# Kernel optimization log

Hardware: AMD Instinct MI355X
Metric: run time of the kernel (lower is better)

## Reference

```python
import jax, jax.numpy as jnp
import numpy as np

B, C, T, H, NCLS = 512, 22, 1000, 64, 4


def setup_inputs() -> dict:
    key = jax.random.key(0)
    ks = jax.random.split(key, 8)
    s_ih = 1.0 / np.sqrt(H)
    x = jax.random.normal(ks[0], (B, C, T), dtype=jnp.float32)
    # PyTorch LSTM params: gate order [i, f, g, o], each of size H
    W_ih = jax.random.uniform(ks[1], (4 * H, C), minval=-s_ih, maxval=s_ih, dtype=jnp.float32)
    W_hh = jax.random.uniform(ks[2], (4 * H, H), minval=-s_ih, maxval=s_ih, dtype=jnp.float32)
    b_ih = jax.random.uniform(ks[3], (4 * H,), minval=-s_ih, maxval=s_ih, dtype=jnp.float32)
    b_hh = jax.random.uniform(ks[4], (4 * H,), minval=-s_ih, maxval=s_ih, dtype=jnp.float32)
    s_fc = 1.0 / np.sqrt(H * T)
    W_fc = jax.random.uniform(ks[5], (NCLS, H * T), minval=-s_fc, maxval=s_fc, dtype=jnp.float32)
    b_fc = jax.random.uniform(ks[6], (NCLS,), minval=-s_fc, maxval=s_fc, dtype=jnp.float32)
    return {"x": x, "W_ih": W_ih, "W_hh": W_hh, "b_ih": b_ih, "b_hh": b_hh,
            "W_fc": W_fc, "b_fc": b_fc}


def _lstm(xs, W_ih, W_hh, b_ih, b_hh):
    # xs: [B, T, C] -> outputs [B, T, H]
    b = xs.shape[0]
    # precompute input projections for all timesteps: [T, B, 4H]
    x_proj = jnp.einsum('btc,gc->tbg', xs, W_ih) + (b_ih + b_hh)
    h0 = jnp.zeros((b, W_hh.shape[1]), xs.dtype)
    c0 = jnp.zeros_like(h0)

    def step(carry, xp):
        h, c = carry
        gates = xp + h @ W_hh.T  # [B, 4H]
        i, f, g, o = jnp.split(gates, 4, axis=-1)
        i = jax.nn.sigmoid(i)
        f = jax.nn.sigmoid(f)
        g = jnp.tanh(g)
        o = jax.nn.sigmoid(o)
        c = f * c + i * g
        h = o * jnp.tanh(c)
        return (h, c), h

    _, hs = jax.lax.scan(step, (h0, c0), x_proj)  # hs: [T, B, H]
    return jnp.transpose(hs, (1, 0, 2))  # [B, T, H]


def reference(x, W_ih, W_hh, b_ih, b_hh, W_fc, b_fc):
    xs = jnp.transpose(x, (0, 2, 1))  # [B, T, C]  (permute(0,2,1))
    hs = _lstm(xs, W_ih, W_hh, b_ih, b_hh)  # [B, T, H]
    flat = hs.reshape(hs.shape[0], -1)  # [B, T*H], time-major per row
    logits = flat @ W_fc.T + b_fc  # [B, 4]
    return jax.nn.softmax(logits, axis=1)
```

## Files before the change

### kernel.cpp

```cpp
#include <hip/hip_runtime.h>

#define BB   512
#define CC   22
#define TT   1000
#define HH   64
#define NCLS 4
#define TC   250
#define NCHUNK (TT / TC)
#define XROW 12

typedef _Float16 f16;
typedef __attribute__((ext_vector_type(2))) _Float16 h2;

__device__ __forceinline__ float sigm(float x) {
    return 1.0f / (1.0f + __expf(-x));
}
__device__ __forceinline__ float tanh_(float x) {
    float e = __expf(-2.0f * fabsf(x));
    float r = (1.0f - e) / (1.0f + e);
    return copysignf(r, x);
}

__device__ __forceinline__ h2 u2h(unsigned u) {
    union { unsigned u; h2 h; } c; c.u = u; return c.h;
}
__device__ __forceinline__ unsigned h2u(h2 h) {
    union { unsigned u; h2 h; } c; c.h = h; return c.u;
}

__global__ __launch_bounds__(64, 1) void lstm_wave(
    const float* __restrict__ x,
    const float* __restrict__ W_ih,
    const float* __restrict__ W_hh,
    const float* __restrict__ b_ih,
    const float* __restrict__ b_hh,
    const float* __restrict__ W_fc,
    const float* __restrict__ b_fc,
    float* __restrict__ out)
{
    __shared__ __align__(16) h2  xs[TC][XROW];
    __shared__ __align__(16) f16 hbuf[HH];

    const int lane = threadIdx.x;
    const int r    = blockIdx.x;

    unsigned whh[4][32];
    unsigned wih[4][11];
    float bias[4];
    #pragma unroll
    for (int g = 0; g < 4; ++g) {
        const int row = g * HH + lane;
        const float* wr = W_hh + row * HH;
        #pragma unroll
        for (int k = 0; k < 32; ++k)
            whh[g][k] = h2u(h2{(f16)wr[2 * k], (f16)wr[2 * k + 1]});
        const float* wi = W_ih + row * CC;
        #pragma unroll
        for (int k = 0; k < 11; ++k)
            wih[g][k] = h2u(h2{(f16)wi[2 * k], (f16)wi[2 * k + 1]});
        bias[g] = b_ih[row] + b_hh[row];
    }
    #pragma unroll
    for (int g = 0; g < 4; ++g) {
        #pragma unroll
        for (int k = 0; k < 32; ++k) asm volatile("" : "+v"(whh[g][k]));
        #pragma unroll
        for (int k = 0; k < 11; ++k) asm volatile("" : "+v"(wih[g][k]));
        asm volatile("" : "+v"(bias[g]));
    }

    hbuf[lane] = (f16)0.0f;
    float c = 0.0f;
    float fc0 = 0.f, fc1 = 0.f, fc2 = 0.f, fc3 = 0.f;
    const float* p0 = W_fc + 0 * (TT * HH) + lane;
    const float* p1 = W_fc + 1 * (TT * HH) + lane;
    const float* p2 = W_fc + 2 * (TT * HH) + lane;
    const float* p3 = W_fc + 3 * (TT * HH) + lane;
    const float* xrow = x + (size_t)r * (CC * TT);

    for (int chunk = 0; chunk < NCHUNK; ++chunk) {
        for (int tb = 0; tb < TC; tb += 64) {
            const int t = tb + lane;
            if (t < TC) {
                const float* gx = xrow + chunk * TC + t;
                union { h2 h[XROW]; uint4 q[3]; } U;
                #pragma unroll
                for (int k = 0; k < 11; ++k)
                    U.h[k] = h2{(f16)gx[(2 * k) * TT], (f16)gx[(2 * k + 1) * TT]};
                U.h[11] = h2{(f16)0.0f, (f16)0.0f};
                uint4* dst = (uint4*)&xs[t][0];
                dst[0] = U.q[0]; dst[1] = U.q[1]; dst[2] = U.q[2];
            }
        }

        for (int tt = 0; tt < TC; ++tt) {
            union { uint4 q[8]; h2 h[32]; } H;
            const uint4* hr = (const uint4*)hbuf;
            #pragma unroll
            for (int i = 0; i < 8; ++i) H.q[i] = hr[i];

            union { uint4 q[3]; h2 h[XROW]; } X;
            const uint4* xr = (const uint4*)&xs[tt][0];
            X.q[0] = xr[0]; X.q[1] = xr[1]; X.q[2] = xr[2];

            float w0 = *p0, w1 = *p1, w2 = *p2, w3 = *p3;
            p0 += HH; p1 += HH; p2 += HH; p3 += HH;

            float a0 = bias[0], a1 = bias[1], a2 = bias[2], a3 = bias[3];
            #pragma unroll
            for (int k = 0; k < 11; ++k) {
                a0 = __builtin_amdgcn_fdot2(X.h[k], u2h(wih[0][k]), a0, false);
                a1 = __builtin_amdgcn_fdot2(X.h[k], u2h(wih[1][k]), a1, false);
                a2 = __builtin_amdgcn_fdot2(X.h[k], u2h(wih[2][k]), a2, false);
                a3 = __builtin_amdgcn_fdot2(X.h[k], u2h(wih[3][k]), a3, false);
            }
            #pragma unroll
            for (int k = 0; k < 32; ++k) {
                a0 = __builtin_amdgcn_fdot2(H.h[k], u2h(whh[0][k]), a0, false);
                a1 = __builtin_amdgcn_fdot2(H.h[k], u2h(whh[1][k]), a1, false);
                a2 = __builtin_amdgcn_fdot2(H.h[k], u2h(whh[2][k]), a2, false);
                a3 = __builtin_amdgcn_fdot2(H.h[k], u2h(whh[3][k]), a3, false);
            }

            float iv = sigm(a0), fv = sigm(a1), gv = tanh_(a2), ov = sigm(a3);
            c = fv * c + iv * gv;
            float h = ov * tanh_(c);

            fc0 += h * w0; fc1 += h * w1; fc2 += h * w2; fc3 += h * w3;

            hbuf[lane] = (f16)h;
        }
    }

    #pragma unroll
    for (int off = 32; off; off >>= 1) {
        fc0 += __shfl_down(fc0, off);
        fc1 += __shfl_down(fc1, off);
        fc2 += __shfl_down(fc2, off);
        fc3 += __shfl_down(fc3, off);
    }
    if (lane == 0) {
        float l0 = fc0 + b_fc[0], l1 = fc1 + b_fc[1];
        float l2 = fc2 + b_fc[2], l3 = fc3 + b_fc[3];
        float m  = fmaxf(fmaxf(l0, l1), fmaxf(l2, l3));
        float e0 = __expf(l0 - m), e1 = __expf(l1 - m);
        float e2 = __expf(l2 - m), e3 = __expf(l3 - m);
        float s  = e0 + e1 + e2 + e3;
        float4 o; o.x = e0 / s; o.y = e1 / s; o.z = e2 / s; o.w = e3 / s;
        *(float4*)(out + r * NCLS) = o;
    }
}

extern "C" void kernel_launch(void* const* d_in, const int* in_sizes, int n_in,
                              void* d_out, int out_size, void* d_ws, size_t ws_size,
                              hipStream_t stream) {
    const float* x    = (const float*)d_in[0];
    const float* W_ih = (const float*)d_in[1];
    const float* W_hh = (const float*)d_in[2];
    const float* b_ih = (const float*)d_in[3];
    const float* b_hh = (const float*)d_in[4];
    const float* W_fc = (const float*)d_in[5];
    const float* b_fc = (const float*)d_in[6];
    float* out = (float*)d_out;

    lstm_wave<<<BB, 64, 0, stream>>>(x, W_ih, W_hh, b_ih, b_hh, W_fc, b_fc, out);
}
```

Measured before the change: 681.1 us.

## Batch 16 sequences per block and compute LSTM gates with MFMA

Replaces the one-wave-per-sequence fdot2 kernel with 256-thread blocks, each handling 16 batch rows. The gate matmul (W_hh and W_ih concatenated as K=96) runs as 16x16x32 f16 MFMAs, with h exchanged through double-buffered LDS and a block barrier every timestep. It also swaps divides for rcp in the activations and reduces the FC partials across waves via LDS. Only 32 blocks are launched, so most CUs sit idle, and the per-step __syncthreads adds latency to the serial recurrence.

```diff
diff --git a/kernel.cpp b/kernel.cpp
--- a/kernel.cpp
+++ b/kernel.cpp
@@ -5,30 +5,35 @@
 #define TT   1000
 #define HH   64
 #define NCLS 4
-#define TC   250
+#define RPB  16
+#define NBLK (BB / RPB)
+#define TC   50
 #define NCHUNK (TT / TC)
-#define XROW 12
+#define FCW  (TT * HH)
 
 typedef _Float16 f16;
 typedef __attribute__((ext_vector_type(2))) _Float16 h2;
+typedef __attribute__((ext_vector_type(8))) _Float16 f16x8;
+typedef __attribute__((ext_vector_type(4))) float    f32x4;
+
+union U16x8 { uint4 q; f16x8 h; f16 e[8]; };
 
 __device__ __forceinline__ float sigm(float x) {
-    return 1.0f / (1.0f + __expf(-x));
+    float e = __expf(-x);
+    return __builtin_amdgcn_rcpf(1.0f + e);
 }
 __device__ __forceinline__ float tanh_(float x) {
     float e = __expf(-2.0f * fabsf(x));
-    float r = (1.0f - e) / (1.0f + e);
+    float r = (1.0f - e) * __builtin_amdgcn_rcpf(1.0f + e);
     return copysignf(r, x);
 }
-
-__device__ __forceinline__ h2 u2h(unsigned u) {
-    union { unsigned u; h2 h; } c; c.u = u; return c.h;
-}
-__device__ __forceinline__ unsigned h2u(h2 h) {
-    union { unsigned u; h2 h; } c; c.h = h; return c.u;
-}
-
-__global__ __launch_bounds__(64, 1) void lstm_wave(
+__device__ __forceinline__ unsigned pack2(float a, float b) {
+    union { unsigned u; h2 h; } c;
+    c.h = h2{(f16)a, (f16)b};
+    return c.u;
+}
+
+__global__ __launch_bounds__(256, 1) void lstm_mfma(
     const float* __restrict__ x,
     const float* __restrict__ W_ih,
     const float* __restrict__ W_hh,
@@ -38,116 +43,151 @@
     const float* __restrict__ b_fc,
     float* __restrict__ out)
 {
-    __shared__ __align__(16) h2  xs[TC][XROW];
-    __shared__ __align__(16) f16 hbuf[HH];
-
-    const int lane = threadIdx.x;
-    const int r    = blockIdx.x;
-
-    unsigned whh[4][32];
-    unsigned wih[4][11];
-    float bias[4];
+    __shared__ uint4 xs[TC * 64];
+    __shared__ uint4 hb[2 * 128];
+    __shared__ float fcp[4][RPB][NCLS];
+
+    const int tid   = threadIdx.x;
+    const int w     = tid >> 6;
+    const int l     = tid & 63;
+    const int c     = l & 15;
+    const int q     = l >> 4;
+    const int hid0  = 16 * w + 4 * q;
+    const int rbase = blockIdx.x * RPB;
+
+    f16x8 wA[4][3];
+    f32x4 biasf[4];
     #pragma unroll
     for (int g = 0; g < 4; ++g) {
-        const int row = g * HH + lane;
-        const float* wr = W_hh + row * HH;
-        #pragma unroll
-        for (int k = 0; k < 32; ++k)
-            whh[g][k] = h2u(h2{(f16)wr[2 * k], (f16)wr[2 * k + 1]});
-        const float* wi = W_ih + row * CC;
-        #pragma unroll
-        for (int k = 0; k < 11; ++k)
-            wih[g][k] = h2u(h2{(f16)wi[2 * k], (f16)wi[2 * k + 1]});
-        bias[g] = b_ih[row] + b_hh[row];
+        const int row = 64 * g + 16 * w + c;
+        const float* whr = W_hh + row * HH;
+        const float* wir = W_ih + row * CC;
+        #pragma unroll
+        for (int kt = 0; kt < 3; ++kt) {
+            U16x8 u;
+            #pragma unroll
+            for (int e = 0; e < 8; ++e) {
+                const int k = 32 * kt + 8 * q + e;
+                float v = 0.0f;
+                if (k < HH) v = whr[k];
+                else if (k < HH + CC) v = wir[k - HH];
+                u.e[e] = (f16)v;
+            }
+            wA[g][kt] = u.h;
+        }
+        const float4 bi = *(const float4*)(b_ih + 64 * g + hid0);
+        const float4 bh = *(const float4*)(b_hh + 64 * g + hid0);
+        biasf[g][0] = bi.x + bh.x; biasf[g][1] = bi.y + bh.y;
+        biasf[g][2] = bi.z + bh.z; biasf[g][3] = bi.w + bh.w;
     }
     #pragma unroll
-    for (int g = 0; g < 4; ++g) {
-        #pragma unroll
-        for (int k = 0; k < 32; ++k) asm volatile("" : "+v"(whh[g][k]));
-        #pragma unroll
-        for (int k = 0; k < 11; ++k) asm volatile("" : "+v"(wih[g][k]));
-        asm volatile("" : "+v"(bias[g]));
-    }
-
-    hbuf[lane] = (f16)0.0f;
-    float c = 0.0f;
-    float fc0 = 0.f, fc1 = 0.f, fc2 = 0.f, fc3 = 0.f;
-    const float* p0 = W_fc + 0 * (TT * HH) + lane;
-    const float* p1 = W_fc + 1 * (TT * HH) + lane;
-    const float* p2 = W_fc + 2 * (TT * HH) + lane;
-    const float* p3 = W_fc + 3 * (TT * HH) + lane;
-    const float* xrow = x + (size_t)r * (CC * TT);
+    for (int g = 0; g < 4; ++g)
+        #pragma unroll
+        for (int kt = 0; kt < 3; ++kt)
+            asm volatile("" : "+v"(wA[g][kt]));
+
+    hb[tid] = uint4{0u, 0u, 0u, 0u};
+
+    float cst[4] = {0.f, 0.f, 0.f, 0.f};
+    float fca[4] = {0.f, 0.f, 0.f, 0.f};
+
+    const int woff = (w >> 1) * 1024 + (2 * (w & 1) + (q >> 1)) * 256
+                   + c * 16 + (q & 1) * 8;
 
     for (int chunk = 0; chunk < NCHUNK; ++chunk) {
-        for (int tb = 0; tb < TC; tb += 64) {
-            const int t = tb + lane;
-            if (t < TC) {
-                const float* gx = xrow + chunk * TC + t;
-                union { h2 h[XROW]; uint4 q[3]; } U;
+        const int T0 = chunk * TC;
+        for (int s = tid; s < TC * 64; s += 256) {
+            const int t  = s >> 6, sl = s & 63;
+            const int sc = sl & 15, sq = sl >> 4;
+            U16x8 u;
+            if (sq == 3) {
+                u.q = uint4{0u, 0u, 0u, 0u};
+            } else {
+                const float* gx = x + (size_t)(rbase + sc) * (CC * TT) + T0 + t;
                 #pragma unroll
-                for (int k = 0; k < 11; ++k)
-                    U.h[k] = h2{(f16)gx[(2 * k) * TT], (f16)gx[(2 * k + 1) * TT]};
-                U.h[11] = h2{(f16)0.0f, (f16)0.0f};
-                uint4* dst = (uint4*)&xs[t][0];
-                dst[0] = U.q[0]; dst[1] = U.q[1]; dst[2] = U.q[2];
+                for (int e = 0; e < 8; ++e) {
+                    const int ch = 8 * sq + e;
+                    u.e[e] = (f16)(ch < CC ? gx[ch * TT] : 0.0f);
+                }
             }
+            xs[s] = u.q;
         }
+        __syncthreads();
 
         for (int tt = 0; tt < TC; ++tt) {
-            union { uint4 q[8]; h2 h[32]; } H;
-            const uint4* hr = (const uint4*)hbuf;
+            const int tg = T0 + tt;
+
+            const float* wp = W_fc + tg * HH + hid0;
+            const float4 wf0 = *(const float4*)(wp);
+            const float4 wf1 = *(const float4*)(wp + FCW);
+            const float4 wf2 = *(const float4*)(wp + 2 * FCW);
+            const float4 wf3 = *(const float4*)(wp + 3 * FCW);
+
+            U16x8 hx0, hx1, xb;
+            const int rb = (tt & 1) * 128;
+            hx0.q = hb[rb + l];
+            hx1.q = hb[rb + 64 + l];
+            xb.q  = xs[tt * 64 + l];
+
+            f32x4 d0 = __builtin_amdgcn_mfma_f32_16x16x32_f16(wA[0][0], hx0.h, biasf[0], 0, 0, 0);
+            f32x4 d1 = __builtin_amdgcn_mfma_f32_16x16x32_f16(wA[1][0], hx0.h, biasf[1], 0, 0, 0);
+            f32x4 d2 = __builtin_amdgcn_mfma_f32_16x16x32_f16(wA[2][0], hx0.h, biasf[2], 0, 0, 0);
+            f32x4 d3 = __builtin_amdgcn_mfma_f32_16x16x32_f16(wA[3][0], hx0.h, biasf[3], 0, 0, 0);
+            d0 = __builtin_amdgcn_mfma_f32_16x16x32_f16(wA[0][1], hx1.h, d0, 0, 0, 0);
+            d1 = __builtin_amdgcn_mfma_f32_16x16x32_f16(wA[1][1], hx1.h, d1, 0, 0, 0);
+            d2 = __builtin_amdgcn_mfma_f32_16x16x32_f16(wA[2][1], hx1.h, d2, 0, 0, 0);
+            d3 = __builtin_amdgcn_mfma_f32_16x16x32_f16(wA[3][1], hx1.h, d3, 0, 0, 0);
+            d0 = __builtin_amdgcn_mfma_f32_16x16x32_f16(wA[0][2], xb.h, d0, 0, 0, 0);
+            d1 = __builtin_amdgcn_mfma_f32_16x16x32_f16(wA[1][2], xb.h, d1, 0, 0, 0);
+            d2 = __builtin_amdgcn_mfma_f32_16x16x32_f16(wA[2][2], xb.h, d2, 0, 0, 0);
+            d3 = __builtin_amdgcn_mfma_f32_16x16x32_f16(wA[3][2], xb.h, d3, 0, 0, 0);
+
+            float h[4];
             #pragma unroll
-            for (int i = 0; i < 8; ++i) H.q[i] = hr[i];
-
-            union { uint4 q[3]; h2 h[XROW]; } X;
-            const uint4* xr = (const uint4*)&xs[tt][0];
-            X.q[0] = xr[0]; X.q[1] = xr[1]; X.q[2] = xr[2];
-
-            float w0 = *p0, w1 = *p1, w2 = *p2, w3 = *p3;
-            p0 += HH; p1 += HH; p2 += HH; p3 += HH;
-
-            float a0 = bias[0], a1 = bias[1], a2 = bias[2], a3 = bias[3];
-            #pragma unroll
-            for (int k = 0; k < 11; ++k) {
-                a0 = __builtin_amdgcn_fdot2(X.h[k], u2h(wih[0][k]), a0, false);
-                a1 = __builtin_amdgcn_fdot2(X.h[k], u2h(wih[1][k]), a1, false);
-                a2 = __builtin_amdgcn_fdot2(X.h[k], u2h(wih[2][k]), a2, false);
-                a3 = __builtin_amdgcn_fdot2(X.h[k], u2h(wih[3][k]), a3, false);
+            for (int r = 0; r < 4; ++r) {
+                const float iv = sigm(d0[r]);
+                const float fv = sigm(d1[r]);
+                const float gv = tanh_(d2[r]);
+                const float ov = sigm(d3[r]);
+                cst[r] = fv * cst[r] + iv * gv;
+                h[r] = ov * tanh_(cst[r]);
             }
-            #pragma unroll
-            for (int k = 0; k < 32; ++k) {
-                a0 = __builtin_amdgcn_fdot2(H.h[k], u2h(whh[0][k]), a0, false);
-                a1 = __builtin_amdgcn_fdot2(H.h[k], u2h(whh[1][k]), a1, false);
-                a2 = __builtin_amdgcn_fdot2(H.h[k], u2h(whh[2][k]), a2, false);
-                a3 = __builtin_amdgcn_fdot2(H.h[k], u2h(whh[3][k]), a3, false);
-            }
-
-            float iv = sigm(a0), fv = sigm(a1), gv = tanh_(a2), ov = sigm(a3);
-            c = fv * c + iv * gv;
-            float h = ov * tanh_(c);
-
-            fc0 += h * w0; fc1 += h * w1; fc2 += h * w2; fc3 += h * w3;
-
-            hbuf[lane] = (f16)h;
+
+            fca[0] += h[0] * wf0.x + h[1] * wf0.y + h[2] * wf0.z + h[3] * wf0.w;
+            fca[1] += h[0] * wf1.x + h[1] * wf1.y + h[2] * wf1.z + h[3] * wf1.w;
+            fca[2] += h[0] * wf2.x + h[1] * wf2.y + h[2] * wf2.z + h[3] * wf2.w;
+            fca[3] += h[0] * wf3.x + h[1] * wf3.y + h[2] * wf3.z + h[3] * wf3.w;
+
+            uint2 hp;
+            hp.x = pack2(h[0], h[1]);
+            hp.y = pack2(h[2], h[3]);
+            *(uint2*)((char*)hb + ((tt + 1) & 1) * 2048 + woff) = hp;
+            __syncthreads();
         }
     }
 
     #pragma unroll
-    for (int off = 32; off; off >>= 1) {
-        fc0 += __shfl_down(fc0, off);
-        fc1 += __shfl_down(fc1, off);
-        fc2 += __shfl_down(fc2, off);
-        fc3 += __shfl_down(fc3, off);
-    }
-    if (lane == 0) {
-        float l0 = fc0 + b_fc[0], l1 = fc1 + b_fc[1];
-        float l2 = fc2 + b_fc[2], l3 = fc3 + b_fc[3];
-        float m  = fmaxf(fmaxf(l0, l1), fmaxf(l2, l3));
-        float e0 = __expf(l0 - m), e1 = __expf(l1 - m);
-        float e2 = __expf(l2 - m), e3 = __expf(l3 - m);
-        float s  = e0 + e1 + e2 + e3;
-        float4 o; o.x = e0 / s; o.y = e1 / s; o.z = e2 / s; o.w = e3 / s;
-        *(float4*)(out + r * NCLS) = o;
+    for (int k = 0; k < 4; ++k) {
+        fca[k] += __shfl_xor(fca[k], 16);
+        fca[k] += __shfl_xor(fca[k], 32);
+    }
+    if (q == 0) {
+        #pragma unroll
+        for (int k = 0; k < 4; ++k) fcp[w][c][k] = fca[k];
+    }
+    __syncthreads();
+    if (w == 0 && l < 16) {
+        float lg[4];
+        #pragma unroll
+        for (int k = 0; k < 4; ++k)
+            lg[k] = fcp[0][l][k] + fcp[1][l][k] + fcp[2][l][k] + fcp[3][l][k]
+                  + b_fc[k];
+        const float m  = fmaxf(fmaxf(lg[0], lg[1]), fmaxf(lg[2], lg[3]));
+        const float e0 = __expf(lg[0] - m), e1 = __expf(lg[1] - m);
+        const float e2 = __expf(lg[2] - m), e3 = __expf(lg[3] - m);
+        const float is = __builtin_amdgcn_rcpf(e0 + e1 + e2 + e3);
+        float4 o; o.x = e0 * is; o.y = e1 * is; o.z = e2 * is; o.w = e3 * is;
+        *(float4*)(out + (rbase + l) * NCLS) = o;
     }
 }
 
@@ -163,5 +203,5 @@
     const float* b_fc = (const float*)d_in[6];
     float* out = (float*)d_out;
 
-    lstm_wave<<<BB, 64, 0, stream>>>(x, W_ih, W_hh, b_ih, b_hh, W_fc, b_fc, out);
-}
+    lstm_mfma<<<NBLK, 256, 0, stream>>>(x, W_ih, W_hh, b_ih, b_hh, W_fc, b_fc, out);
+}
```

Result: slower. 850.8 us (+24.9%).
